# Optimization experiments

Measured on AMD Instinct MI355X. Metric: run time of the kernel, lower is better.

The kernel has to match this reference:

```python
import jax, jax.numpy as jnp
import numpy as np

DIM = 192
NH = 6
HD = DIM // NH            # 32
SCALE = HD ** -0.5
HID = int(DIM * 4.0)      # 768
EPS = 1e-5


def _ln(x, g, b):
    m = jnp.mean(x, axis=-1, keepdims=True)
    v = jnp.mean((x - m) ** 2, axis=-1, keepdims=True)
    return (x - m) * jax.lax.rsqrt(v + EPS) * g + b


def setup_inputs() -> dict:
    key = jax.random.key(0)
    ks = jax.random.split(key, 6)
    H = W = T = 48
    B = 1
    L = H * W * T
    return {
        "x": jax.random.normal(ks[0], (B, L, DIM), jnp.float32),
        "norm1_g": jnp.ones((DIM,), jnp.float32),
        "norm1_b": jnp.zeros((DIM,), jnp.float32),
        "qkv_w": jax.random.normal(ks[1], (3 * DIM, DIM), jnp.float32) * 0.02,
        "qkv_b": jnp.zeros((3 * DIM,), jnp.float32),
        "proj_w": jax.random.normal(ks[2], (DIM, DIM), jnp.float32) * 0.02,
        "proj_b": jnp.zeros((DIM,), jnp.float32),
        "norm2_g": jnp.ones((DIM,), jnp.float32),
        "norm2_b": jnp.zeros((DIM,), jnp.float32),
        "fc1_w": jax.random.normal(ks[3], (HID, DIM), jnp.float32) * 0.02,
        "fc1_b": jnp.zeros((HID,), jnp.float32),
        "fc2_w": jax.random.normal(ks[4], (DIM, HID), jnp.float32) * 0.02,
        "fc2_b": jnp.zeros((DIM,), jnp.float32),
        "H": H, "W": W, "T": T,
    }


def reference(x, norm1_g, norm1_b, qkv_w, qkv_b, proj_w, proj_b,
              norm2_g, norm2_b, fc1_w, fc1_b, fc2_w, fc2_b, H, W, T):
    B, L, C = x.shape
    shortcut = x
    h = _ln(x, norm1_g, norm1_b)
    # axial_dims='12' -> extra_dim=3: permute to (B, T, H, W, C), attend over H*W
    h = h.reshape(B, H, W, T, C).transpose(0, 3, 1, 2, 4).reshape(B * T, H * W, C)
    B_, N, _ = h.shape
    qkv = h @ qkv_w.T + qkv_b                                   # (B_, N, 3C)
    # faithful reproduction of the module's unusual reshape mixing batch into head dim
    qkv = qkv.transpose(1, 0, 2).reshape(1, N, 3, NH, B_ * HD).transpose(2, 0, 3, 1, 4)
    q, k, v = qkv[0] * SCALE, qkv[1], qkv[2]                    # (1, NH, N, B_*HD)
    attn = jax.nn.softmax(jnp.einsum('ohnd,ohmd->ohnm', q, k), axis=-1)
    o = jnp.einsum('ohnm,ohmd->ohnd', attn, v)                  # (1, NH, N, B_*HD)
    o = o.transpose(0, 2, 1, 3).reshape(B_, N, C)
    o = o @ proj_w.T + proj_b
    o = o.reshape(B, H * W * T, C)                              # module does NOT undo the permute
    x1 = shortcut + o
    m = _ln(x1, norm2_g, norm2_b)
    m = jax.nn.gelu(m @ fc1_w.T + fc1_b, approximate=False) @ fc2_w.T + fc2_b
    return x1 + m
```

## Files before the change

### kernel.cpp

```cpp
#include <hip/hip_runtime.h>

typedef __bf16 bf16_t;
typedef __attribute__((ext_vector_type(8))) __bf16 bf16x8;
typedef __attribute__((ext_vector_type(4))) float f32x4;

__device__ __forceinline__ float gelu_exact(float x) {
    return 0.5f * x * (1.0f + erff(x * 0.70710678118654752f));
}

template<int BM, int BN, int EPI, int SWZ>
__global__ __launch_bounds__(256)
void mgemm(const bf16_t* __restrict__ A, int lda, long aBatch,
           const bf16_t* __restrict__ B, int ldb, long bBatch,
           bf16_t* __restrict__ C, int ldc, long cBatch,
           const float* __restrict__ bias, int K,
           float* __restrict__ Cf, const float* __restrict__ resid)
{
    constexpr int MR = BM / 32;
    constexpr int NR = BN / 32;
    __shared__ __align__(16) bf16_t As[BM * 32];
    __shared__ __align__(16) bf16_t Bs[BN * 32];
    const int t    = threadIdx.x;
    const int w    = t >> 6;
    const int lane = t & 63;
    const int wr   = w >> 1, wc = w & 1;

    unsigned bx = blockIdx.x, by = blockIdx.y, bz = blockIdx.z;
    if constexpr (SWZ) {
        const unsigned gx = gridDim.x, gy = gridDim.y, gz = gridDim.z;
        unsigned lin = (bz * gy + by) * gx + bx;
        const unsigned cpx = (gx * gy * gz) >> 3;
        lin = (lin & 7) * cpx + (lin >> 3);
        bx = lin % gx; lin /= gx;
        by = lin % gy; bz = lin / gy;
    }

    const long n0 = (long)bx * BN;
    const long m0 = (long)by * BM;
    A += (long)bz * aBatch;
    B += (long)bz * bBatch;
    if constexpr (EPI != 3) C += (long)bz * cBatch;

    f32x4 acc[MR][NR] = {};

    const int sr = t >> 2;
    const int sc = (t & 3) * 8;
    const int kq   = (lane >> 4) * 8;
    const int lrow = lane & 15;

    for (int k0 = 0; k0 < K; k0 += 32) {
        #pragma unroll
        for (int c = 0; c < BM / 64; ++c) {
            const bf16_t* src = A + (m0 + c * 64 + sr) * (long)lda + (k0 + sc);
            __builtin_amdgcn_global_load_lds(
                (__attribute__((address_space(1))) void*)(bf16_t*)src,
                (__attribute__((address_space(3))) void*)(As + c * 2048 + w * 512),
                16, 0, 0);
        }
        #pragma unroll
        for (int c = 0; c < BN / 64; ++c) {
            const bf16_t* src = B + (n0 + c * 64 + sr) * (long)ldb + (k0 + sc);
            __builtin_amdgcn_global_load_lds(
                (__attribute__((address_space(1))) void*)(bf16_t*)src,
                (__attribute__((address_space(3))) void*)(Bs + c * 2048 + w * 512),
                16, 0, 0);
        }
        __syncthreads();

        bf16x8 af[MR], bfr[NR];
        #pragma unroll
        for (int i = 0; i < MR; ++i)
            af[i] = *(const bf16x8*)(As + (wr * (BM / 2) + i * 16 + lrow) * 32 + kq);
        #pragma unroll
        for (int j = 0; j < NR; ++j)
            bfr[j] = *(const bf16x8*)(Bs + (wc * (BN / 2) + j * 16 + lrow) * 32 + kq);
        #pragma unroll
        for (int i = 0; i < MR; ++i)
            #pragma unroll
            for (int j = 0; j < NR; ++j)
                acc[i][j] = __builtin_amdgcn_mfma_f32_16x16x32_bf16(af[i], bfr[j], acc[i][j], 0, 0, 0);
        __syncthreads();
    }

    const int ccol  = lane & 15;
    const int crow4 = (lane >> 4) * 4;
    #pragma unroll
    for (int i = 0; i < MR; ++i) {
        long rowb = m0 + wr * (BM / 2) + i * 16 + crow4;
        #pragma unroll
        for (int j = 0; j < NR; ++j) {
            long col = n0 + wc * (BN / 2) + j * 16 + ccol;
            #pragma unroll
            for (int r = 0; r < 4; ++r) {
                float v = acc[i][j][r];
                long row = rowb + r;
                if constexpr (EPI == 0) {
                    C[row * ldc + col] = (bf16_t)v;
                } else if constexpr (EPI == 1) {
                    C[row * ldc + col] = (bf16_t)(v + bias[col]);
                } else if constexpr (EPI == 2) {
                    C[row * ldc + col] = (bf16_t)gelu_exact(v + bias[col]);
                } else {
                    long idx = row * ldc + col;
                    Cf[idx] = resid[idx] + v + bias[col];
                }
            }
        }
    }
}

__global__ __launch_bounds__(256)
void transpose_v(const bf16_t* __restrict__ Y, bf16_t* __restrict__ Vt)
{
    __shared__ bf16_t tile[64][80];
    const int h  = blockIdx.z;
    const int e0 = blockIdx.x * 64;
    const int m0 = blockIdx.y * 64;
    const int t  = threadIdx.x;
    const int lr = t >> 3;
    const int lc8 = t & 7;

    #pragma unroll
    for (int i = 0; i < 64; i += 32) {
        int row = lr + i;
        bf16x8 vv = *(const bf16x8*)(Y + (long)(m0 + row) * 27648 + 18432 + h * 1536 + e0 + lc8 * 8);
        int cs = lc8 ^ (row >> 3);
        *(bf16x8*)&tile[row][cs * 8] = vv;
    }
    __syncthreads();
    #pragma unroll
    for (int i = 0; i < 64; i += 32) {
        int er = lr + i;
        bf16x8 vv;
        #pragma unroll
        for (int j = 0; j < 8; ++j) {
            int row = lc8 * 8 + j;
            int cs = (er >> 3) ^ lc8;
            vv[j] = tile[row][cs * 8 + (er & 7)];
        }
        *(bf16x8*)(Vt + ((long)h * 1536 + e0 + er) * 2304 + m0 + lc8 * 8) = vv;
    }
}

__global__ __launch_bounds__(256)
void ln_fast(const float* __restrict__ x, const float* __restrict__ g,
             const float* __restrict__ b, bf16_t* __restrict__ o, int nrows)
{
    const int lane = threadIdx.x & 63;
    const int wave = threadIdx.x >> 6;
    const float g0 = g[lane], g1 = g[lane + 64], g2 = g[lane + 128];
    const float b0 = b[lane], b1 = b[lane + 64], b2 = b[lane + 128];
    for (long row = (long)blockIdx.x * 4 + wave; row < nrows; row += (long)gridDim.x * 4) {
        const float* xr = x + row * 192;
        float v0 = xr[lane], v1 = xr[lane + 64], v2 = xr[lane + 128];
        float s  = v0 + v1 + v2;
        float ss = v0 * v0 + v1 * v1 + v2 * v2;
        #pragma unroll
        for (int d = 32; d > 0; d >>= 1) {
            s  += __shfl_xor(s, d);
            ss += __shfl_xor(ss, d);
        }
        float mean = s * (1.f / 192.f);
        float var  = ss * (1.f / 192.f) - mean * mean;
        float rs   = rsqrtf(var + 1e-5f);
        bf16_t* orow = o + row * 192;
        orow[lane]       = (bf16_t)((v0 - mean) * rs * g0 + b0);
        orow[lane + 64]  = (bf16_t)((v1 - mean) * rs * g1 + b1);
        orow[lane + 128] = (bf16_t)((v2 - mean) * rs * g2 + b2);
    }
}

__global__ __launch_bounds__(256)
void softmax_fast(bf16_t* __restrict__ S)
{
    const float SC = 0.17677669529663687f;
    __shared__ float wmax[4], wsum[4];
    const long base = (long)blockIdx.x * 2304;
    const int t = threadIdx.x;
    const int lane = t & 63, w = t >> 6;
    float v[9];
    float mx = -1e30f;
    #pragma unroll
    for (int i = 0; i < 9; ++i) {
        v[i] = (float)S[base + t + i * 256] * SC;
        mx = fmaxf(mx, v[i]);
    }
    #pragma unroll
    for (int d = 32; d > 0; d >>= 1) mx = fmaxf(mx, __shfl_xor(mx, d));
    if (lane == 0) wmax[w] = mx;
    __syncthreads();
    mx = fmaxf(fmaxf(wmax[0], wmax[1]), fmaxf(wmax[2], wmax[3]));
    float sum = 0.f;
    #pragma unroll
    for (int i = 0; i < 9; ++i) { v[i] = __expf(v[i] - mx); sum += v[i]; }
    #pragma unroll
    for (int d = 32; d > 0; d >>= 1) sum += __shfl_xor(sum, d);
    if (lane == 0) wsum[w] = sum;
    __syncthreads();
    const float inv = 1.f / (wsum[0] + wsum[1] + wsum[2] + wsum[3]);
    #pragma unroll
    for (int i = 0; i < 9; ++i) S[base + t + i * 256] = (bf16_t)(v[i] * inv);
}

__global__ __launch_bounds__(256)
void cast_wq(const float* __restrict__ w, int n, bf16_t* __restrict__ o)
{
    int i = blockIdx.x * 256 + threadIdx.x;
    if (i < n) o[i] = (bf16_t)w[i];
}

extern "C" void kernel_launch(void* const* d_in, const int* in_sizes, int n_in,
                              void* d_out, int out_size, void* d_ws, size_t ws_size,
                              hipStream_t stream)
{
    (void)in_sizes; (void)n_in; (void)out_size; (void)ws_size;
    const float* x      = (const float*)d_in[0];
    const float* n1g    = (const float*)d_in[1];
    const float* n1b    = (const float*)d_in[2];
    const float* qkv_w  = (const float*)d_in[3];
    const float* qkv_b  = (const float*)d_in[4];
    const float* proj_w = (const float*)d_in[5];
    const float* proj_b = (const float*)d_in[6];
    const float* n2g    = (const float*)d_in[7];
    const float* n2b    = (const float*)d_in[8];
    const float* fc1_w  = (const float*)d_in[9];
    const float* fc1_b  = (const float*)d_in[10];
    const float* fc2_w  = (const float*)d_in[11];
    const float* fc2_b  = (const float*)d_in[12];
    float* out = (float*)d_out;

    char* ws = (char*)d_ws;
    size_t off = 0;
    auto alloc = [&](size_t nbytes) -> void* {
        off = (off + 255) & ~(size_t)255;
        void* p = ws + off;
        off += nbytes;
        return p;
    };

    bf16_t* Wq   = (bf16_t*)alloc((size_t)576 * 192 * 2);
    bf16_t* Wp   = (bf16_t*)alloc((size_t)192 * 192 * 2);
    bf16_t* W1   = (bf16_t*)alloc((size_t)768 * 192 * 2);
    bf16_t* W2   = (bf16_t*)alloc((size_t)192 * 768 * 2);
    bf16_t* Hbuf = (bf16_t*)alloc((size_t)110592 * 192 * 2);
    bf16_t* Qkv  = (bf16_t*)alloc((size_t)110592 * 768 * 2);
    bf16_t* Vt   = Qkv + (size_t)110592 * 576;
    bf16_t* Sbuf = (bf16_t*)d_out;

    cast_wq<<<432, 256, 0, stream>>>(qkv_w, 576 * 192, Wq);
    cast_wq<<<144, 256, 0, stream>>>(proj_w, 192 * 192, Wp);
    cast_wq<<<576, 256, 0, stream>>>(fc1_w, 768 * 192, W1);
    cast_wq<<<576, 256, 0, stream>>>(fc2_w, 192 * 768, W2);

    ln_fast<<<2048, 256, 0, stream>>>(x, n1g, n1b, Hbuf, 110592);
    mgemm<128, 64, 1, 0><<<dim3(9, 864, 1), 256, 0, stream>>>(
        Hbuf, 192, 0, Wq, 192, 0, Qkv, 576, 0, qkv_b, 192, nullptr, nullptr);
    transpose_v<<<dim3(24, 36, 6), 256, 0, stream>>>(Qkv, Vt);
    mgemm<128, 128, 0, 1><<<dim3(18, 18, 6), 256, 0, stream>>>(
        Qkv, 27648, 1536, Qkv + 9216, 27648, 1536,
        Sbuf, 2304, (long)2304 * 2304, nullptr, 1536, nullptr, nullptr);
    softmax_fast<<<13824, 256, 0, stream>>>(Sbuf);
    mgemm<128, 128, 0, 1><<<dim3(12, 18, 6), 256, 0, stream>>>(
        Sbuf, 2304, (long)2304 * 2304, Vt, 2304, (long)1536 * 2304,
        Hbuf, 9216, 1536, nullptr, 2304, nullptr, nullptr);
    mgemm<128, 64, 3, 0><<<dim3(3, 864, 1), 256, 0, stream>>>(
        Hbuf, 192, 0, Wp, 192, 0, nullptr, 192, 0, proj_b, 192, out, x);
    ln_fast<<<2048, 256, 0, stream>>>(out, n2g, n2b, Hbuf, 110592);
    mgemm<128, 128, 2, 0><<<dim3(6, 864, 1), 256, 0, stream>>>(
        Hbuf, 192, 0, W1, 192, 0, Qkv, 768, 0, fc1_b, 192, nullptr, nullptr);
    mgemm<128, 64, 3, 0><<<dim3(3, 864, 1), 256, 0, stream>>>(
        Qkv, 768, 0, W2, 768, 0, nullptr, 192, 0, fc2_b, 768, out, out);
}
```

Before: 830.2 us.

## Double GEMM K-tile to 64 with XOR-swizzled LDS layout; merge weight casts

Raises the GEMM K step from 32 to 64, so each tile loads twice as much data per barrier pair and issues twice as many MFMAs between syncs. The LDS layout gains an XOR swizzle on 16-byte chunks to avoid bank conflicts on the fragment reads. The four weight-cast launches are merged into one kernel to cut launch overhead. In exchange the kernel uses twice the LDS, which may lower occupancy, and it now requires K to be a multiple of 64, which holds for 192, 768, 1536 and 2304.

Result: no change. 820.0 us (-1.2%).

```diff
diff --git a/kernel.cpp b/kernel.cpp
--- a/kernel.cpp
+++ b/kernel.cpp
@@ -18,8 +18,8 @@
 {
     constexpr int MR = BM / 32;
     constexpr int NR = BN / 32;
-    __shared__ __align__(16) bf16_t As[BM * 32];
-    __shared__ __align__(16) bf16_t Bs[BN * 32];
+    __shared__ __align__(16) bf16_t As[BM * 64];
+    __shared__ __align__(16) bf16_t Bs[BN * 64];
     const int t    = threadIdx.x;
     const int w    = t >> 6;
     const int lane = t & 63;
@@ -43,23 +43,23 @@
 
     f32x4 acc[MR][NR] = {};
 
-    const int sr = t >> 2;
-    const int sc = (t & 3) * 8;
-    const int kq   = (lane >> 4) * 8;
+    const int srow8 = t >> 3;
+    const int schunk = (t & 7) ^ (srow8 & 7);
     const int lrow = lane & 15;
-
-    for (int k0 = 0; k0 < K; k0 += 32) {
-        #pragma unroll
-        for (int c = 0; c < BM / 64; ++c) {
-            const bf16_t* src = A + (m0 + c * 64 + sr) * (long)lda + (k0 + sc);
+    const int kq4  = lane >> 4;
+
+    for (int k0 = 0; k0 < K; k0 += 64) {
+        #pragma unroll
+        for (int c = 0; c < BM / 32; ++c) {
+            const bf16_t* src = A + (m0 + c * 32 + srow8) * (long)lda + (k0 + schunk * 8);
             __builtin_amdgcn_global_load_lds(
                 (__attribute__((address_space(1))) void*)(bf16_t*)src,
                 (__attribute__((address_space(3))) void*)(As + c * 2048 + w * 512),
                 16, 0, 0);
         }
         #pragma unroll
-        for (int c = 0; c < BN / 64; ++c) {
-            const bf16_t* src = B + (n0 + c * 64 + sr) * (long)ldb + (k0 + sc);
+        for (int c = 0; c < BN / 32; ++c) {
+            const bf16_t* src = B + (n0 + c * 32 + srow8) * (long)ldb + (k0 + schunk * 8);
             __builtin_amdgcn_global_load_lds(
                 (__attribute__((address_space(1))) void*)(bf16_t*)src,
                 (__attribute__((address_space(3))) void*)(Bs + c * 2048 + w * 512),
@@ -67,18 +67,33 @@
         }
         __syncthreads();
 
-        bf16x8 af[MR], bfr[NR];
-        #pragma unroll
-        for (int i = 0; i < MR; ++i)
-            af[i] = *(const bf16x8*)(As + (wr * (BM / 2) + i * 16 + lrow) * 32 + kq);
-        #pragma unroll
-        for (int j = 0; j < NR; ++j)
-            bfr[j] = *(const bf16x8*)(Bs + (wc * (BN / 2) + j * 16 + lrow) * 32 + kq);
-        #pragma unroll
-        for (int i = 0; i < MR; ++i)
-            #pragma unroll
-            for (int j = 0; j < NR; ++j)
-                acc[i][j] = __builtin_amdgcn_mfma_f32_16x16x32_bf16(af[i], bfr[j], acc[i][j], 0, 0, 0);
+        bf16x8 af[MR][2], bfr[NR][2];
+        #pragma unroll
+        for (int i = 0; i < MR; ++i) {
+            const int row = wr * (BM / 2) + i * 16 + lrow;
+            #pragma unroll
+            for (int ks = 0; ks < 2; ++ks) {
+                const int ch = (ks * 4 + kq4) ^ (row & 7);
+                af[i][ks] = *(const bf16x8*)(As + row * 64 + ch * 8);
+            }
+        }
+        #pragma unroll
+        for (int j = 0; j < NR; ++j) {
+            const int row = wc * (BN / 2) + j * 16 + lrow;
+            #pragma unroll
+            for (int ks = 0; ks < 2; ++ks) {
+                const int ch = (ks * 4 + kq4) ^ (row & 7);
+                bfr[j][ks] = *(const bf16x8*)(Bs + row * 64 + ch * 8);
+            }
+        }
+        #pragma unroll
+        for (int ks = 0; ks < 2; ++ks)
+            #pragma unroll
+            for (int i = 0; i < MR; ++i)
+                #pragma unroll
+                for (int j = 0; j < NR; ++j)
+                    acc[i][j] = __builtin_amdgcn_mfma_f32_16x16x32_bf16(
+                        af[i][ks], bfr[j][ks], acc[i][j], 0, 0, 0);
         __syncthreads();
     }
 
@@ -203,10 +218,16 @@
 }
 
 __global__ __launch_bounds__(256)
-void cast_wq(const float* __restrict__ w, int n, bf16_t* __restrict__ o)
+void cast_all(const float* __restrict__ w0, const float* __restrict__ w1,
+              const float* __restrict__ w2, const float* __restrict__ w3,
+              bf16_t* __restrict__ o0, bf16_t* __restrict__ o1,
+              bf16_t* __restrict__ o2, bf16_t* __restrict__ o3)
 {
     int i = blockIdx.x * 256 + threadIdx.x;
-    if (i < n) o[i] = (bf16_t)w[i];
+    if (i < 110592)       o0[i] = (bf16_t)w0[i];
+    else if (i < 147456)  o1[i - 110592] = (bf16_t)w1[i - 110592];
+    else if (i < 294912)  o2[i - 147456] = (bf16_t)w2[i - 147456];
+    else if (i < 442368)  o3[i - 294912] = (bf16_t)w3[i - 294912];
 }
 
 extern "C" void kernel_launch(void* const* d_in, const int* in_sizes, int n_in,
@@ -247,10 +268,7 @@
     bf16_t* Vt   = Qkv + (size_t)110592 * 576;
     bf16_t* Sbuf = (bf16_t*)d_out;
 
-    cast_wq<<<432, 256, 0, stream>>>(qkv_w, 576 * 192, Wq);
-    cast_wq<<<144, 256, 0, stream>>>(proj_w, 192 * 192, Wp);
-    cast_wq<<<576, 256, 0, stream>>>(fc1_w, 768 * 192, W1);
-    cast_wq<<<576, 256, 0, stream>>>(fc2_w, 192 * 768, W2);
+    cast_all<<<1728, 256, 0, stream>>>(qkv_w, proj_w, fc1_w, fc2_w, Wq, Wp, W1, W2);
 
     ln_fast<<<2048, 256, 0, stream>>>(x, n1g, n1b, Hbuf, 110592);
     mgemm<128, 64, 1, 0><<<dim3(9, 864, 1), 256, 0, stream>>>(
```
